# Performance work log

Measured on AMD Instinct MI355X. Metric: run time of the kernel, lower is better.

Reference implementation:

```python
import jax, jax.numpy as jnp
import numpy as np

N_ENT = 100000
D = 128
N_EDGES = 1600000
B = 8192
EPS = 1e-5


def setup_inputs() -> dict:
    key = jax.random.key(0)
    ks = jax.random.split(key, 12)
    return {
        "E": jax.random.normal(ks[0], (N_ENT, D), jnp.float32),
        "gamma": jnp.ones((D,), jnp.float32),
        "beta": jnp.zeros((D,), jnp.float32),
        "W_gnn": jax.random.normal(ks[1], (D, D), jnp.float32) / np.sqrt(D),
        "b_gnn": jnp.zeros((D,), jnp.float32),
        "W_g": jax.random.normal(ks[2], (D,), jnp.float32) / np.sqrt(D),
        "b_g": jnp.zeros((), jnp.float32),
        "W_age": jax.random.normal(ks[3], (D, 7), jnp.float32) / np.sqrt(D),
        "b_age": jnp.zeros((7,), jnp.float32),
        "W_occ": jax.random.normal(ks[4], (D, 21), jnp.float32) / np.sqrt(D),
        "b_occ": jnp.zeros((21,), jnp.float32),
        "src": jax.random.randint(ks[5], (N_EDGES,), 0, N_ENT, jnp.int32),
        "dst": jax.random.randint(ks[6], (N_EDGES,), 0, N_ENT, jnp.int32),
        "neighbor": jax.random.randint(ks[7], (B,), 0, N_ENT, jnp.int32),
        "gender": jax.random.randint(ks[8], (B,), 0, 2, jnp.int32),
        "age": jax.random.randint(ks[9], (B,), 0, 7, jnp.int32),
        "occupation": jax.random.randint(ks[10], (B,), 0, 21, jnp.int32),
    }


def reference(E, gamma, beta, W_gnn, b_gnn, W_g, b_g, W_age, b_age, W_occ, b_occ,
              src, dst, neighbor, gender, age, occupation):
    n = E.shape[0]
    # encoder (embedding of all nodes) -> batchnorm over node axis
    mu = jnp.mean(E, axis=0)
    var = jnp.var(E, axis=0)
    h = (E - mu) * jax.lax.rsqrt(var + EPS) * gamma + beta  # [N, D]
    # gnn: mean neighbor aggregation over edge list, then linear + relu
    agg = jax.ops.segment_sum(h[src], dst, num_segments=n)  # [N, D]
    deg = jax.ops.segment_sum(jnp.ones_like(src, jnp.float32), dst, num_segments=n)
    agg = agg / jnp.maximum(deg, 1.0)[:, None]
    h = jax.nn.relu(agg @ W_gnn + b_gnn)  # [N, D]
    # gather walked-to nodes; gradient-reversal layer is identity in forward
    u = h[neighbor]  # [B, D]
    gender_pred = u @ W_g + b_g            # [B]
    age_pred = u @ W_age + b_age           # [B, 7]
    occ_pred = u @ W_occ + b_occ           # [B, 21]
    # mode == 'gender': BCEWithLogitsLoss (mean)
    z = gender.astype(jnp.float32)
    x = gender_pred
    loss_adv = jnp.mean(jnp.maximum(x, 0.0) - x * z + jnp.log1p(jnp.exp(-jnp.abs(x))))
    return (loss_adv, age_pred, gender_pred, occ_pred)
```

## Files before the change

### kernel.cpp

```cpp
#include <hip/hip_runtime.h>
#include <math.h>

#define N_ENT   100000
#define DIM     128
#define N_EDGES 1600000
#define BATCH   8192
#define EPS     1e-5f
#define CAP     64
#define NSTAT_BLK 512
#define HW_LD   132

#define WS_SCALE     256
#define WS_SHIFT     384
#define WS_BCOUNT    528
#define WS_SLOTOF    8720
#define WS_BUCKET    108720
#define WS_PARTIAL   633008
#define WS_EBF       764080

__device__ __forceinline__ unsigned bfpack(float a, float b) {
    unsigned ua = __float_as_uint(a);
    unsigned ub = __float_as_uint(b);
    ua = (ua + 0x7FFFu + ((ua >> 16) & 1u)) >> 16;
    ub = (ub + 0x7FFFu + ((ub >> 16) & 1u)) & 0xFFFF0000u;
    return ua | ub;
}
__device__ __forceinline__ float bflo(unsigned u) { return __uint_as_float(u << 16); }
__device__ __forceinline__ float bfhi(unsigned u) { return __uint_as_float(u & 0xFFFF0000u); }

__global__ __launch_bounds__(256) void stats_init_kernel(const float4* __restrict__ E4,
                                                         const int* __restrict__ neighbor,
                                                         int* __restrict__ slot_of,
                                                         int* __restrict__ bcount,
                                                         uint2* __restrict__ ebf2,
                                                         float* __restrict__ out_loss,
                                                         float* __restrict__ partial) {
    int t = threadIdx.x;
    if (blockIdx.x >= NSTAT_BLK) {
        int n = (blockIdx.x - NSTAT_BLK) * 256 + t;
        if (n < BATCH) {
            bcount[n] = 0;
            slot_of[neighbor[n]] = n;
        }
        if (n == 0) out_loss[0] = 0.f;
        return;
    }
    int sid = blockIdx.x;
    int cg = t & 31;
    int rs = t >> 5;
    const int STRIDE = NSTAT_BLK * 8;
    float sx = 0.f, sy = 0.f, sz = 0.f, sw = 0.f;
    float qx = 0.f, qy = 0.f, qz = 0.f, qw = 0.f;
    const float4 z4 = make_float4(0.f, 0.f, 0.f, 0.f);
    for (int r = sid * 8 + rs; r < N_ENT; r += 8 * STRIDE) {
        float4 v[8];
        int rr[8];
#pragma unroll
        for (int k = 0; k < 8; ++k) {
            rr[k] = r + k * STRIDE;
            v[k] = (rr[k] < N_ENT) ? E4[(size_t)rr[k] * 32 + cg] : z4;
        }
#pragma unroll
        for (int k = 0; k < 8; ++k) {
            if (rr[k] < N_ENT) {
                uint2 p;
                p.x = bfpack(v[k].x, v[k].y);
                p.y = bfpack(v[k].z, v[k].w);
                ebf2[(size_t)rr[k] * 32 + cg] = p;
            }
            sx += v[k].x; sy += v[k].y; sz += v[k].z; sw += v[k].w;
            qx += v[k].x * v[k].x; qy += v[k].y * v[k].y;
            qz += v[k].z * v[k].z; qw += v[k].w * v[k].w;
        }
    }
    __shared__ float sh[8 * 256];
    sh[0 * 256 + t] = sx; sh[1 * 256 + t] = sy;
    sh[2 * 256 + t] = sz; sh[3 * 256 + t] = sw;
    sh[4 * 256 + t] = qx; sh[5 * 256 + t] = qy;
    sh[6 * 256 + t] = qz; sh[7 * 256 + t] = qw;
    __syncthreads();
    for (int o = 128; o >= 32; o >>= 1) {
        if (t < o) {
#pragma unroll
            for (int j = 0; j < 8; ++j) sh[j * 256 + t] += sh[j * 256 + t + o];
        }
        __syncthreads();
    }
    if (t < 32) {
#pragma unroll
        for (int j = 0; j < 8; ++j)
            partial[sid * 256 + j * 32 + t] = sh[j * 256 + t];
    }
}

__global__ __launch_bounds__(256) void edge_finalize_kernel(const int4* __restrict__ src4,
                                                            const int4* __restrict__ dst4,
                                                            const int* __restrict__ slot_of,
                                                            int* __restrict__ bcount,
                                                            int* __restrict__ bucket,
                                                            const float* __restrict__ partial,
                                                            const float* __restrict__ gamma,
                                                            const float* __restrict__ beta,
                                                            float* __restrict__ scale,
                                                            float* __restrict__ shift) {
    if (blockIdx.x == 0) {
        int t = threadIdx.x;
        float s = 0.f;
#pragma unroll 16
        for (int b = 0; b < NSTAT_BLK; ++b) s += partial[b * 256 + t];
        __shared__ float tot[256];
        tot[t] = s;
        __syncthreads();
        if (t < 128) {
            int ti = t >> 2, j = t & 3;
            const float invn = 1.0f / (float)N_ENT;
            float mu = tot[j * 32 + ti] * invn;
            float var = tot[(j + 4) * 32 + ti] * invn - mu * mu;
            float rs = rsqrtf(var + EPS);
            float sc = gamma[t] * rs;
            scale[t] = sc;
            shift[t] = beta[t] - mu * sc;
        }
        return;
    }
    const int n4 = N_EDGES / 4;
    int tid = (blockIdx.x - 1) * blockDim.x + threadIdx.x;
    int e0 = tid * 2;
    int e1 = tid * 2 + 1;
    if (e0 >= n4) return;
    int4 d0 = dst4[e0];
    int4 s0 = src4[e0];
    bool has1 = (e1 < n4);
    int4 d1 = has1 ? dst4[e1] : make_int4(0, 0, 0, 0);
    int4 s1 = has1 ? src4[e1] : make_int4(0, 0, 0, 0);
    int sl0 = slot_of[d0.x];
    int sl1 = slot_of[d0.y];
    int sl2 = slot_of[d0.z];
    int sl3 = slot_of[d0.w];
    int sl4 = has1 ? slot_of[d1.x] : -1;
    int sl5 = has1 ? slot_of[d1.y] : -1;
    int sl6 = has1 ? slot_of[d1.z] : -1;
    int sl7 = has1 ? slot_of[d1.w] : -1;
    if (sl0 >= 0) { int p = atomicAdd(&bcount[sl0], 1); if (p < CAP) bucket[sl0 * CAP + p] = s0.x; }
    if (sl1 >= 0) { int p = atomicAdd(&bcount[sl1], 1); if (p < CAP) bucket[sl1 * CAP + p] = s0.y; }
    if (sl2 >= 0) { int p = atomicAdd(&bcount[sl2], 1); if (p < CAP) bucket[sl2 * CAP + p] = s0.z; }
    if (sl3 >= 0) { int p = atomicAdd(&bcount[sl3], 1); if (p < CAP) bucket[sl3 * CAP + p] = s0.w; }
    if (sl4 >= 0) { int p = atomicAdd(&bcount[sl4], 1); if (p < CAP) bucket[sl4 * CAP + p] = s1.x; }
    if (sl5 >= 0) { int p = atomicAdd(&bcount[sl5], 1); if (p < CAP) bucket[sl5 * CAP + p] = s1.y; }
    if (sl6 >= 0) { int p = atomicAdd(&bcount[sl6], 1); if (p < CAP) bucket[sl6 * CAP + p] = s1.z; }
    if (sl7 >= 0) { int p = atomicAdd(&bcount[sl7], 1); if (p < CAP) bucket[sl7 * CAP + p] = s1.w; }
}

__global__ __launch_bounds__(256) void item_fused_kernel(const uint4* __restrict__ ebf4,
                                                         const int* __restrict__ neighbor,
                                                         const int* __restrict__ gender,
                                                         const int* __restrict__ slot_of,
                                                         const int* __restrict__ bcount,
                                                         const int* __restrict__ bucket,
                                                         const float* __restrict__ scale,
                                                         const float* __restrict__ shift,
                                                         const float4* __restrict__ W4,
                                                         const float4* __restrict__ bias4,
                                                         const float* __restrict__ W_g,
                                                         const float* __restrict__ b_g,
                                                         const float* __restrict__ W_age,
                                                         const float* __restrict__ b_age,
                                                         const float* __restrict__ W_occ,
                                                         const float* __restrict__ b_occ,
                                                         float* __restrict__ out_age,
                                                         float* __restrict__ out_gender,
                                                         float* __restrict__ out_occ,
                                                         float* __restrict__ out_loss) {
    __shared__ __align__(16) float A_s[8 * 128];
    __shared__ __align__(16) float HW[29 * HW_LD];
    __shared__ float sh[256];
    __shared__ float hb[32];
    __shared__ int   cslot_s[8];
    const int t = threadIdx.x;
    const int item0 = blockIdx.x * 8;

    if (t < 8) cslot_s[t] = slot_of[neighbor[item0 + t]];
    for (int idx = t; idx < 29 * 128; idx += 256) {
        int h = idx >> 7;
        int d = idx & 127;
        float v;
        if (h < 7)       v = W_age[d * 7 + h];
        else if (h < 28) v = W_occ[d * 21 + (h - 7)];
        else             v = W_g[d];
        HW[h * HW_LD + d] = v;
    }
    if (t < 29) hb[t] = (t < 7) ? b_age[t] : (t < 28) ? b_occ[t - 7] : b_g[0];
    __syncthreads();

    {
        const int lane = t & 63;
        const int q  = lane & 15;
        const int es = (lane >> 4) & 1;
        const int li = t >> 5;
        int cs = cslot_s[li];
        int dg = bcount[cs];
        int m = dg < CAP ? dg : CAP;
        const int* bk = bucket + cs * CAP;
        float a0 = 0.f, a1 = 0.f, a2 = 0.f, a3 = 0.f;
        float a4 = 0.f, a5 = 0.f, a6 = 0.f, a7 = 0.f;
        int ib = 0;
        for (; ib + 15 < m; ib += 16) {
            int e0 = ib + es;
            int r0 = bk[e0],      r1 = bk[e0 + 2],  r2 = bk[e0 + 4],  r3 = bk[e0 + 6];
            int r4 = bk[e0 + 8],  r5 = bk[e0 + 10], r6 = bk[e0 + 12], r7 = bk[e0 + 14];
            uint4 v0 = ebf4[(size_t)r0 * 16 + q];
            uint4 v1 = ebf4[(size_t)r1 * 16 + q];
            uint4 v2 = ebf4[(size_t)r2 * 16 + q];
            uint4 v3 = ebf4[(size_t)r3 * 16 + q];
            uint4 v4 = ebf4[(size_t)r4 * 16 + q];
            uint4 v5 = ebf4[(size_t)r5 * 16 + q];
            uint4 v6 = ebf4[(size_t)r6 * 16 + q];
            uint4 v7 = ebf4[(size_t)r7 * 16 + q];
#define ACC(V) do { \
            a0 += bflo(V.x); a1 += bfhi(V.x); a2 += bflo(V.y); a3 += bfhi(V.y); \
            a4 += bflo(V.z); a5 += bfhi(V.z); a6 += bflo(V.w); a7 += bfhi(V.w); } while (0)
            ACC(v0); ACC(v1); ACC(v2); ACC(v3); ACC(v4); ACC(v5); ACC(v6); ACC(v7);
        }
        for (int e = ib + es; e < m; e += 2) {
            int r0 = bk[e];
            uint4 v0 = ebf4[(size_t)r0 * 16 + q];
            ACC(v0);
        }
#undef ACC
        a0 += __shfl_down(a0, 16); a1 += __shfl_down(a1, 16);
        a2 += __shfl_down(a2, 16); a3 += __shfl_down(a3, 16);
        a4 += __shfl_down(a4, 16); a5 += __shfl_down(a5, 16);
        a6 += __shfl_down(a6, 16); a7 += __shfl_down(a7, 16);
        if (es == 0) {
            float4* dst = (float4*)(A_s + li * 128 + q * 8);
            dst[0] = make_float4(a0, a1, a2, a3);
            dst[1] = make_float4(a4, a5, a6, a7);
        }
    }
    __syncthreads();

    const int row = t >> 5;
    const int c4  = t & 31;
    {
        int cs = cslot_s[row];
        float fdg = (float)bcount[cs];
        float rd = 1.0f / fmaxf(fdg, 1.0f);
        float4 v = ((float4*)A_s)[row * 32 + c4];
        float4 sc = ((const float4*)scale)[c4];
        float4 sf = ((const float4*)shift)[c4];
        float4 o;
        o.x = (v.x * sc.x + fdg * sf.x) * rd;
        o.y = (v.y * sc.y + fdg * sf.y) * rd;
        o.z = (v.z * sc.z + fdg * sf.z) * rd;
        o.w = (v.w * sc.w + fdg * sf.w) * rd;
        ((float4*)A_s)[row * 32 + c4] = o;
    }
    __syncthreads();

    {
        float a0 = 0.f, a1 = 0.f, a2 = 0.f, a3 = 0.f;
#pragma unroll 4
        for (int k = 0; k < 128; ++k) {
            float a = A_s[row * 128 + k];
            float4 wv = W4[k * 32 + c4];
            a0 += a * wv.x; a1 += a * wv.y; a2 += a * wv.z; a3 += a * wv.w;
        }
        float4 bv = bias4[c4];
        __syncthreads();
        float4 o2;
        o2.x = fmaxf(a0 + bv.x, 0.f);
        o2.y = fmaxf(a1 + bv.y, 0.f);
        o2.z = fmaxf(a2 + bv.z, 0.f);
        o2.w = fmaxf(a3 + bv.w, 0.f);
        ((float4*)A_s)[row * 32 + c4] = o2;
    }
    __syncthreads();

    float val = 0.f;
    if (c4 < 29) {
        const float4* h4 = (const float4*)(A_s + row * 128);
        const float4* w4 = (const float4*)(HW + c4 * HW_LD);
        float b0 = hb[c4], b1 = 0.f, b2 = 0.f, b3 = 0.f;
#pragma unroll 8
        for (int dd = 0; dd < 32; ++dd) {
            float4 hv = h4[dd];
            float4 wv = w4[dd];
            b0 += hv.x * wv.x;
            b1 += hv.y * wv.y;
            b2 += hv.z * wv.z;
            b3 += hv.w * wv.w;
        }
        float x = b0 + b1 + b2 + b3;
        int item = item0 + row;
        if (c4 < 7)       out_age[item * 7 + c4] = x;
        else if (c4 < 28) out_occ[item * 21 + (c4 - 7)] = x;
        else {
            out_gender[item] = x;
            float z = (float)gender[item];
            val = fmaxf(x, 0.f) - x * z + log1pf(expf(-fabsf(x)));
        }
    }
    sh[t] = val;
    __syncthreads();
    for (int o = 128; o > 0; o >>= 1) {
        if (t < o) sh[t] += sh[t + o];
        __syncthreads();
    }
    if (t == 0) atomicAdd(out_loss, sh[0] * (1.0f / (float)BATCH));
}

extern "C" void kernel_launch(void* const* d_in, const int* in_sizes, int n_in,
                              void* d_out, int out_size, void* d_ws, size_t ws_size,
                              hipStream_t stream) {
    const float* E      = (const float*)d_in[0];
    const float* gamma  = (const float*)d_in[1];
    const float* beta   = (const float*)d_in[2];
    const float* W_gnn  = (const float*)d_in[3];
    const float* b_gnn  = (const float*)d_in[4];
    const float* W_g    = (const float*)d_in[5];
    const float* b_g    = (const float*)d_in[6];
    const float* W_age  = (const float*)d_in[7];
    const float* b_age  = (const float*)d_in[8];
    const float* W_occ  = (const float*)d_in[9];
    const float* b_occ  = (const float*)d_in[10];
    const int*   src    = (const int*)d_in[11];
    const int*   dst    = (const int*)d_in[12];
    const int*   neigh  = (const int*)d_in[13];
    const int*   gender = (const int*)d_in[14];

    float* ws  = (float*)d_ws;
    int*   wsi = (int*)d_ws;
    float* scale   = ws + WS_SCALE;
    float* shift   = ws + WS_SHIFT;
    int*   bcount  = wsi + WS_BCOUNT;
    int*   slot_of = wsi + WS_SLOTOF;
    int*   bucket  = wsi + WS_BUCKET;
    float* partial = ws + WS_PARTIAL;
    unsigned* ebf  = (unsigned*)(wsi + WS_EBF);

    float* out       = (float*)d_out;
    float* out_loss  = out;
    float* out_age   = out + 1;
    float* out_gen   = out + 1 + BATCH * 7;
    float* out_occ   = out + 1 + BATCH * 7 + BATCH;

    stats_init_kernel<<<NSTAT_BLK + BATCH / 256, 256, 0, stream>>>(
        (const float4*)E, neigh, slot_of, bcount, (uint2*)ebf, out_loss, partial);
    {
        const int n4 = N_EDGES / 4;
        int nthreads = (n4 + 1) / 2;
        int eblocks = (nthreads + 255) / 256;
        edge_finalize_kernel<<<1 + eblocks, 256, 0, stream>>>(
            (const int4*)src, (const int4*)dst, slot_of, bcount, bucket,
            partial, gamma, beta, scale, shift);
    }
    item_fused_kernel<<<BATCH / 8, 256, 0, stream>>>(
        (const uint4*)ebf, neigh, gender, slot_of, bcount, bucket, scale, shift,
        (const float4*)W_gnn, (const float4*)b_gnn,
        W_g, b_g, W_age, b_age, W_occ, b_occ,
        out_age, out_gen, out_occ, out_loss);
}
```

Measured before the change: 194.2 us.

## Restructure batch-row GEMV to reuse W across rows and branchless masked gather

The per-item GEMV is reorganised so each thread loads one W float4 per k and applies it to all 8 rows, splitting K across 8 lanes and reducing with shuffles. This cuts redundant global W loads, which were previously repeated for each of the 8 rows. The neighbour gather loop becomes a single fully unrolled loop with clamped indices and bitmask zeroing, replacing the separate tail loop. The shared A buffer is padded to reduce LDS bank conflicts. The trade-off is more registers (32 accumulators) and some wasted loads on partial iterations.

Result: faster. 187.0 us (-3.7%).

```diff
diff --git a/kernel.cpp b/kernel.cpp
--- a/kernel.cpp
+++ b/kernel.cpp
@@ -9,6 +9,7 @@
 #define CAP     64
 #define NSTAT_BLK 512
 #define HW_LD   132
+#define A_LD    132
 
 #define WS_SCALE     256
 #define WS_SHIFT     384
@@ -171,7 +172,7 @@
                                                          float* __restrict__ out_gender,
                                                          float* __restrict__ out_occ,
                                                          float* __restrict__ out_loss) {
-    __shared__ __align__(16) float A_s[8 * 128];
+    __shared__ __align__(16) float A_s[8 * A_LD];
     __shared__ __align__(16) float HW[29 * HW_LD];
     __shared__ float sh[256];
     __shared__ float hb[32];
@@ -203,36 +204,38 @@
         const int* bk = bucket + cs * CAP;
         float a0 = 0.f, a1 = 0.f, a2 = 0.f, a3 = 0.f;
         float a4 = 0.f, a5 = 0.f, a6 = 0.f, a7 = 0.f;
-        int ib = 0;
-        for (; ib + 15 < m; ib += 16) {
-            int e0 = ib + es;
-            int r0 = bk[e0],      r1 = bk[e0 + 2],  r2 = bk[e0 + 4],  r3 = bk[e0 + 6];
-            int r4 = bk[e0 + 8],  r5 = bk[e0 + 10], r6 = bk[e0 + 12], r7 = bk[e0 + 14];
-            uint4 v0 = ebf4[(size_t)r0 * 16 + q];
-            uint4 v1 = ebf4[(size_t)r1 * 16 + q];
-            uint4 v2 = ebf4[(size_t)r2 * 16 + q];
-            uint4 v3 = ebf4[(size_t)r3 * 16 + q];
-            uint4 v4 = ebf4[(size_t)r4 * 16 + q];
-            uint4 v5 = ebf4[(size_t)r5 * 16 + q];
-            uint4 v6 = ebf4[(size_t)r6 * 16 + q];
-            uint4 v7 = ebf4[(size_t)r7 * 16 + q];
-#define ACC(V) do { \
-            a0 += bflo(V.x); a1 += bfhi(V.x); a2 += bflo(V.y); a3 += bfhi(V.y); \
-            a4 += bflo(V.z); a5 += bfhi(V.z); a6 += bflo(V.w); a7 += bfhi(V.w); } while (0)
-            ACC(v0); ACC(v1); ACC(v2); ACC(v3); ACC(v4); ACC(v5); ACC(v6); ACC(v7);
-        }
-        for (int e = ib + es; e < m; e += 2) {
-            int r0 = bk[e];
-            uint4 v0 = ebf4[(size_t)r0 * 16 + q];
-            ACC(v0);
-        }
-#undef ACC
+        int iters = (m + 15) >> 4;
+        int mm1 = m > 0 ? m - 1 : 0;
+        for (int it = 0; it < iters; ++it) {
+            int e0 = it * 16 + es;
+            int rr[8];
+            unsigned ok[8];
+#pragma unroll
+            for (int j = 0; j < 8; ++j) {
+                int e = e0 + 2 * j;
+                int ec = e < mm1 ? e : mm1;
+                rr[j] = bk[ec];
+                ok[j] = (e < m) ? 0xFFFFFFFFu : 0u;
+            }
+            uint4 v[8];
+#pragma unroll
+            for (int j = 0; j < 8; ++j)
+                v[j] = ebf4[(size_t)rr[j] * 16 + q];
+#pragma unroll
+            for (int j = 0; j < 8; ++j) {
+                unsigned mk = ok[j];
+                a0 += bflo(v[j].x & mk); a1 += bfhi(v[j].x & mk);
+                a2 += bflo(v[j].y & mk); a3 += bfhi(v[j].y & mk);
+                a4 += bflo(v[j].z & mk); a5 += bfhi(v[j].z & mk);
+                a6 += bflo(v[j].w & mk); a7 += bfhi(v[j].w & mk);
+            }
+        }
         a0 += __shfl_down(a0, 16); a1 += __shfl_down(a1, 16);
         a2 += __shfl_down(a2, 16); a3 += __shfl_down(a3, 16);
         a4 += __shfl_down(a4, 16); a5 += __shfl_down(a5, 16);
         a6 += __shfl_down(a6, 16); a7 += __shfl_down(a7, 16);
         if (es == 0) {
-            float4* dst = (float4*)(A_s + li * 128 + q * 8);
+            float4* dst = (float4*)(A_s + li * A_LD + q * 8);
             dst[0] = make_float4(a0, a1, a2, a3);
             dst[1] = make_float4(a4, a5, a6, a7);
         }
@@ -245,7 +248,7 @@
         int cs = cslot_s[row];
         float fdg = (float)bcount[cs];
         float rd = 1.0f / fmaxf(fdg, 1.0f);
-        float4 v = ((float4*)A_s)[row * 32 + c4];
+        float4 v = ((float4*)(A_s + row * A_LD))[c4];
         float4 sc = ((const float4*)scale)[c4];
         float4 sf = ((const float4*)shift)[c4];
         float4 o;
@@ -253,32 +256,58 @@
         o.y = (v.y * sc.y + fdg * sf.y) * rd;
         o.z = (v.z * sc.z + fdg * sf.z) * rd;
         o.w = (v.w * sc.w + fdg * sf.w) * rd;
-        ((float4*)A_s)[row * 32 + c4] = o;
+        ((float4*)(A_s + row * A_LD))[c4] = o;
     }
     __syncthreads();
 
     {
-        float a0 = 0.f, a1 = 0.f, a2 = 0.f, a3 = 0.f;
+        const int ks = t & 7;
+        const int cg = t >> 3;
+        float acc[8][4];
+#pragma unroll
+        for (int r = 0; r < 8; ++r) {
+            acc[r][0] = 0.f; acc[r][1] = 0.f; acc[r][2] = 0.f; acc[r][3] = 0.f;
+        }
 #pragma unroll 4
-        for (int k = 0; k < 128; ++k) {
-            float a = A_s[row * 128 + k];
-            float4 wv = W4[k * 32 + c4];
-            a0 += a * wv.x; a1 += a * wv.y; a2 += a * wv.z; a3 += a * wv.w;
-        }
-        float4 bv = bias4[c4];
+        for (int kk = 0; kk < 16; ++kk) {
+            int k = ks + 8 * kk;
+            float4 wv = W4[k * 32 + cg];
+#pragma unroll
+            for (int r = 0; r < 8; ++r) {
+                float a = A_s[r * A_LD + k];
+                acc[r][0] += a * wv.x; acc[r][1] += a * wv.y;
+                acc[r][2] += a * wv.z; acc[r][3] += a * wv.w;
+            }
+        }
+#pragma unroll
+        for (int off = 4; off > 0; off >>= 1) {
+#pragma unroll
+            for (int r = 0; r < 8; ++r) {
+                acc[r][0] += __shfl_down(acc[r][0], off);
+                acc[r][1] += __shfl_down(acc[r][1], off);
+                acc[r][2] += __shfl_down(acc[r][2], off);
+                acc[r][3] += __shfl_down(acc[r][3], off);
+            }
+        }
+        float4 bv = bias4[cg];
         __syncthreads();
-        float4 o2;
-        o2.x = fmaxf(a0 + bv.x, 0.f);
-        o2.y = fmaxf(a1 + bv.y, 0.f);
-        o2.z = fmaxf(a2 + bv.z, 0.f);
-        o2.w = fmaxf(a3 + bv.w, 0.f);
-        ((float4*)A_s)[row * 32 + c4] = o2;
+        if (ks == 0) {
+#pragma unroll
+            for (int r = 0; r < 8; ++r) {
+                float4 o2;
+                o2.x = fmaxf(acc[r][0] + bv.x, 0.f);
+                o2.y = fmaxf(acc[r][1] + bv.y, 0.f);
+                o2.z = fmaxf(acc[r][2] + bv.z, 0.f);
+                o2.w = fmaxf(acc[r][3] + bv.w, 0.f);
+                ((float4*)(A_s + r * A_LD))[cg] = o2;
+            }
+        }
     }
     __syncthreads();
 
     float val = 0.f;
     if (c4 < 29) {
-        const float4* h4 = (const float4*)(A_s + row * 128);
+        const float4* h4 = (const float4*)(A_s + row * A_LD);
         const float4* w4 = (const float4*)(HW + c4 * HW_LD);
         float b0 = hb[c4], b1 = 0.f, b2 = 0.f, b3 = 0.f;
 #pragma unroll 8
```
